# Kernel optimization log

Hardware: AMD Instinct MI355X
Metric: run time of the kernel (lower is better)

## Reference

```python
import jax, jax.numpy as jnp
import numpy as np

HIDDEN = 1024
HEADS = 16
D_K = HIDDEN // HEADS
NEG_INF = -jnp.inf


def setup_inputs() -> dict:
    key = jax.random.key(0)
    ks = jax.random.split(key, 9)
    N, S = 4, 2048
    scale = 1.0 / np.sqrt(HIDDEN)
    x = jax.random.normal(ks[0], (N, S, HIDDEN), dtype=jnp.float32)
    attn_mask = jnp.ones((N, S), dtype=jnp.int32)
    Wq = jax.random.normal(ks[1], (HIDDEN, HIDDEN), dtype=jnp.float32) * scale
    bq = jnp.zeros((HIDDEN,), dtype=jnp.float32)
    Wk = jax.random.normal(ks[2], (HIDDEN, HIDDEN), dtype=jnp.float32) * scale
    bk = jnp.zeros((HIDDEN,), dtype=jnp.float32)
    Wv = jax.random.normal(ks[3], (HIDDEN, HIDDEN), dtype=jnp.float32) * scale
    bv = jnp.zeros((HIDDEN,), dtype=jnp.float32)
    Wp = jax.random.normal(ks[4], (HIDDEN, HIDDEN), dtype=jnp.float32) * scale
    bp = jnp.zeros((HIDDEN,), dtype=jnp.float32)
    return {"x": x, "attn_mask": attn_mask, "Wq": Wq, "bq": bq,
            "Wk": Wk, "bk": bk, "Wv": Wv, "bv": bv, "Wp": Wp, "bp": bp}


def reference(x, attn_mask, Wq, bq, Wk, bk, Wv, bv, Wp, bp):
    N, S, _ = x.shape
    H, dk = HEADS, D_K
    # torch nn.Linear: y = x @ W.T + b
    q = (x @ Wq.T + bq).reshape(N, S, H, dk).transpose(0, 2, 1, 3)  # (N,H,S,dk)
    k = (x @ Wk.T + bk).reshape(N, S, H, dk).transpose(0, 2, 1, 3)
    v = (x @ Wv.T + bv).reshape(N, S, H, dk).transpose(0, 2, 1, 3)
    attn = jnp.einsum('nhqd,nhkd->nhqk', q, k) / jnp.sqrt(jnp.float32(dk))
    mask = attn_mask.reshape(N, 1, 1, S)
    attn = jnp.where(mask == 0, NEG_INF, attn)
    attn = jax.nn.softmax(attn, axis=-1)
    # dropout is identity in eval mode
    y = jnp.einsum('nhqk,nhkd->nhqd', attn, v)  # (N,H,S,dk)
    y = y.transpose(0, 2, 1, 3).reshape(N, S, H * dk)
    return y @ Wp.T + bp
```

## Files before the change

### kernel.cpp

```cpp
#include <hip/hip_runtime.h>

typedef unsigned short u16;
typedef unsigned int u32;
typedef unsigned long long u64;
typedef __attribute__((ext_vector_type(8))) short bf16x8;
typedef __attribute__((ext_vector_type(4))) short bf16x4;
typedef __attribute__((ext_vector_type(4))) float f32x4;
typedef __attribute__((ext_vector_type(2))) unsigned int u32x2;

#define AS1(p) ((const __attribute__((address_space(1))) void*)(p))
#define AS3(p) ((__attribute__((address_space(3))) void*)(p))

__device__ __forceinline__ u16 f2bf(float f) {
    u32 u = __float_as_uint(f);
    u += 0x7fff + ((u >> 16) & 1);
    return (u16)(u >> 16);
}
__device__ __forceinline__ u32 pack2bf(float lo, float hi) {
    u32 a = __float_as_uint(lo) + 0x8000u;
    u32 b = __float_as_uint(hi) + 0x8000u;
    return __builtin_amdgcn_perm(b, a, 0x07060302);
}
__device__ __forceinline__ u32 cvtpk(float lo, float hi) {
    u32 r;
    asm("v_cvt_pk_bf16_f32 %0, %1, %2" : "=v"(r) : "v"(lo), "v"(hi));
    return r;
}

__device__ __forceinline__ void async16(const u16* g, u16* l) {
    __builtin_amdgcn_global_load_lds(AS1(g), AS3(l), 16, 0, 0);
}

__global__ __launch_bounds__(256) void cvt_kernel(const float* __restrict__ src,
                                                  u16* __restrict__ dst, int n) {
    int idx = (blockIdx.x * 256 + threadIdx.x) * 8;
    if (idx >= n) return;
    float4 a = *(const float4*)(src + idx);
    float4 b = *(const float4*)(src + idx + 4);
    uint4 o;
    o.x = (u32)f2bf(a.x) | ((u32)f2bf(a.y) << 16);
    o.y = (u32)f2bf(a.z) | ((u32)f2bf(a.w) << 16);
    o.z = (u32)f2bf(b.x) | ((u32)f2bf(b.y) << 16);
    o.w = (u32)f2bf(b.z) | ((u32)f2bf(b.w) << 16);
    *(uint4*)(dst + idx) = o;
}

__global__ __launch_bounds__(256) void cvt4_kernel(
    const float* __restrict__ s0, const float* __restrict__ s1,
    const float* __restrict__ s2, const float* __restrict__ s3,
    u16* __restrict__ d0, u16* __restrict__ d1,
    u16* __restrict__ d2, u16* __restrict__ d3) {
    const float* s; u16* d;
    switch (blockIdx.y) {
        case 0:  s = s0; d = d0; break;
        case 1:  s = s1; d = d1; break;
        case 2:  s = s2; d = d2; break;
        default: s = s3; d = d3; break;
    }
    int idx = (blockIdx.x * 256 + threadIdx.x) * 8;
    float4 a = *(const float4*)(s + idx);
    float4 b = *(const float4*)(s + idx + 4);
    uint4 o;
    o.x = (u32)f2bf(a.x) | ((u32)f2bf(a.y) << 16);
    o.y = (u32)f2bf(a.z) | ((u32)f2bf(a.w) << 16);
    o.z = (u32)f2bf(b.x) | ((u32)f2bf(b.y) << 16);
    o.w = (u32)f2bf(b.z) | ((u32)f2bf(b.w) << 16);
    *(uint4*)(d + idx) = o;
}

__global__ __launch_bounds__(256, 2) void gemm_bt(
    const u16* __restrict__ A,
    const u16* __restrict__ Wa, const u16* __restrict__ Wb, const u16* __restrict__ Wc,
    const float* __restrict__ ba, const float* __restrict__ bb, const float* __restrict__ bc,
    void* oa, void* ob_, void* oc, int mode)
{
    constexpr int K = 1024;
    __shared__ u16 smem[128 * 132];
    u16* At = smem;
    u16* Wt = smem + 4096;

    const int tid = threadIdx.x;
    const int lane = tid & 63, wv = tid >> 6;
    const int l15 = lane & 15, quad = lane >> 4;
    const int wr = wv >> 1, wc = wv & 1;

    const int L = blockIdx.x + (blockIdx.y << 3) + (blockIdx.z << 9);
    const int g = L & 7;
    const int j = L >> 3;
    const int z = j >> 6;
    const int r = j & 63;
    const int m0 = ((g << 3) + (r & 7)) * 128;
    const int n0 = (r >> 3) * 128;

    const u16* W = (z == 0) ? Wa : ((z == 1) ? Wb : Wc);
    const float* bs = (z == 0) ? ba : ((z == 1) ? bb : bc);
    void* out = (z == 0) ? oa : ((z == 1) ? ob_ : oc);
    const bool swap_ = (mode == 1) || (z < 2);

    f32x4 acc[4][4];
#pragma unroll
    for (int i = 0; i < 4; ++i)
#pragma unroll
        for (int j2 = 0; j2 < 4; ++j2) acc[i][j2] = (f32x4)0.f;

    const int call0 = wv * 2;
    for (int kk = 0; kk < K; kk += 32) {
#pragma unroll
        for (int jj = 0; jj < 2; ++jj) {
            int c = (call0 + jj) * 64 + lane;
            int row = c >> 2;
            int ko = ((c & 3) ^ (row & 3)) * 8;
            async16(A + (size_t)(m0 + row) * K + kk + ko, &At[(call0 + jj) * 512 + lane * 8]);
            async16(W + (size_t)(n0 + row) * K + kk + ko, &Wt[(call0 + jj) * 512 + lane * 8]);
        }
        __syncthreads();

        bf16x8 af[4], wf[4];
#pragma unroll
        for (int t = 0; t < 4; ++t) {
            int rowa = wr * 64 + t * 16 + l15;
            af[t] = *(const bf16x8*)&At[rowa * 32 + ((quad ^ (rowa & 3)) * 8)];
            int rowb = wc * 64 + t * 16 + l15;
            wf[t] = *(const bf16x8*)&Wt[rowb * 32 + ((quad ^ (rowb & 3)) * 8)];
        }
        if (swap_) {
#pragma unroll
            for (int rt = 0; rt < 4; ++rt)
#pragma unroll
                for (int ct = 0; ct < 4; ++ct)
                    acc[rt][ct] = __builtin_amdgcn_mfma_f32_16x16x32_bf16(wf[ct], af[rt], acc[rt][ct], 0, 0, 0);
        } else {
#pragma unroll
            for (int rt = 0; rt < 4; ++rt)
#pragma unroll
                for (int ct = 0; ct < 4; ++ct)
                    acc[rt][ct] = __builtin_amdgcn_mfma_f32_16x16x32_bf16(af[rt], wf[ct], acc[rt][ct], 0, 0, 0);
        }
        __syncthreads();
    }

    if (mode == 1) {
#pragma unroll
        for (int rt = 0; rt < 4; ++rt)
#pragma unroll
            for (int ct = 0; ct < 4; ++ct) {
                int m_ = m0 + wr * 64 + rt * 16 + l15;
                int ob = n0 + wc * 64 + ct * 16 + quad * 4;
                float4 b4 = *(const float4*)&bs[ob];
                float4 v;
                v.x = acc[rt][ct][0] + b4.x;
                v.y = acc[rt][ct][1] + b4.y;
                v.z = acc[rt][ct][2] + b4.z;
                v.w = acc[rt][ct][3] + b4.w;
                *(float4*)((float*)out + (size_t)m_ * 1024 + ob) = v;
            }
        return;
    }

    const int n = m0 >> 11, s0 = m0 & 2047;
    if (z < 2) {
        const float qs = (z == 0) ? 0.18033688011112042f : 1.0f;
#pragma unroll
        for (int rt = 0; rt < 4; ++rt)
#pragma unroll
            for (int ct = 0; ct < 4; ++ct) {
                int ml = wr * 64 + rt * 16 + l15;
                int ol = wc * 64 + ct * 16 + quad * 4;
                float4 b4 = *(const float4*)&bs[n0 + ol];
                float v0 = (acc[rt][ct][0] + b4.x) * qs;
                float v1 = (acc[rt][ct][1] + b4.y) * qs;
                float v2 = (acc[rt][ct][2] + b4.z) * qs;
                float v3 = (acc[rt][ct][3] + b4.w) * qs;
                u32x2 pv = { pack2bf(v0, v1), pack2bf(v2, v3) };
                *(u32x2*)&smem[ml * 132 + ol] = pv;
            }
        __syncthreads();
        const int h0 = n0 >> 6;
#pragma unroll
        for (int p = 0; p < 8; ++p) {
            int hh = p >> 2, qq = p & 3;
            int m = qq * 32 + (tid >> 3), d = (tid & 7) * 8;
            bf16x8 vv = *(const bf16x8*)&smem[m * 132 + hh * 64 + d];
            u16* dst = (u16*)out + ((size_t)((n * 16 + h0 + hh) * 2048 + s0 + m)) * 64 + d;
            *(bf16x8*)dst = vv;
        }
    } else {
#pragma unroll
        for (int rt = 0; rt < 4; ++rt)
#pragma unroll
            for (int ct = 0; ct < 4; ++ct) {
                int ol = wc * 64 + ct * 16 + l15;
                int ml = wr * 64 + rt * 16 + quad * 4;
                float b = bs[n0 + ol];
                float v0 = acc[rt][ct][0] + b;
                float v1 = acc[rt][ct][1] + b;
                float v2 = acc[rt][ct][2] + b;
                float v3 = acc[rt][ct][3] + b;
                u32x2 pv = { pack2bf(v0, v1), pack2bf(v2, v3) };
                *(u32x2*)&smem[ol * 132 + ml] = pv;
            }
        __syncthreads();
#pragma unroll
        for (int p = 0; p < 8; ++p) {
            int o = p * 16 + (tid >> 4), ms = (tid & 15) * 8;
            bf16x8 vv = *(const bf16x8*)&smem[o * 132 + ms];
            int og = n0 + o;
            int h = og >> 6, d = og & 63;
            u16* dst = (u16*)out + ((size_t)((n * 16 + h) * 64 + d)) * 2048 + s0 + ms;
            *(bf16x8*)dst = vv;
        }
    }
}

__global__ __launch_bounds__(256) void attn_kernel(
    const u16* __restrict__ Q, const u16* __restrict__ K_,
    const u16* __restrict__ VT, const int* __restrict__ mask,
    u16* __restrict__ Y)
{
    constexpr int S = 2048, DK = 64, STR = 72;
    __shared__ u16 Kt[64 * STR];
    __shared__ u16 Vt[64 * STR];
    __shared__ int mtile[64];

    const int tid = threadIdx.x;
    const int lane = tid & 63, w = tid >> 6;
    const int l15 = lane & 15, quad = lane >> 4;

    const int L = blockIdx.x + (blockIdx.y << 4);
    const int vb = (L & 7) * 128 + (L >> 3);
    const int nh = vb >> 4;
    const int n = nh >> 4, h = nh & 15;
    const int qbase = (vb & 15) * 128;

    const u16* Qh = Q + (size_t)nh * S * DK;
    const u16* Kh = K_ + (size_t)nh * S * DK;
    const u16* Vh = VT + (size_t)nh * DK * S;

    bf16x8 qf[2][2];
#pragma unroll
    for (int nt = 0; nt < 2; ++nt)
#pragma unroll
        for (int st = 0; st < 2; ++st)
            qf[nt][st] = *(const bf16x8*)(Qh + (size_t)(qbase + w * 32 + nt * 16 + l15) * DK + st * 32 + quad * 8);

    f32x4 o[4][2];
#pragma unroll
    for (int dt = 0; dt < 4; ++dt)
#pragma unroll
        for (int nt = 0; nt < 2; ++nt) o[dt][nt] = (f32x4)0.f;
    float lsum[2] = {0.f, 0.f};

    const int r0 = tid >> 3, c8 = (tid & 7) * 8;
    bf16x8 rk0 = *(const bf16x8*)(Kh + (size_t)r0 * 64 + c8);
    bf16x8 rk1 = *(const bf16x8*)(Kh + (size_t)(r0 + 32) * 64 + c8);
    bf16x8 rv0 = *(const bf16x8*)(Vh + (size_t)r0 * S + c8);
    bf16x8 rv1 = *(const bf16x8*)(Vh + (size_t)(r0 + 32) * S + c8);
    int mreg = 0;
    if (tid < 64) mreg = mask[n * S + tid];

    for (int it = 0; it < 32; ++it) {
        *(bf16x8*)&Kt[r0 * STR + c8] = rk0;
        *(bf16x8*)&Kt[(r0 + 32) * STR + c8] = rk1;
        *(bf16x8*)&Vt[r0 * STR + c8] = rv0;
        *(bf16x8*)&Vt[(r0 + 32) * STR + c8] = rv1;
        if (tid < 64) mtile[tid] = mreg;
        __syncthreads();

        const int kkn = ((it + 1) << 6) & (S - 1);
        rk0 = *(const bf16x8*)(Kh + (size_t)(kkn + r0) * 64 + c8);
        rk1 = *(const bf16x8*)(Kh + (size_t)(kkn + r0 + 32) * 64 + c8);
        rv0 = *(const bf16x8*)(Vh + (size_t)r0 * S + kkn + c8);
        rv1 = *(const bf16x8*)(Vh + (size_t)(r0 + 32) * S + kkn + c8);
        if (tid < 64) mreg = mask[n * S + kkn + tid];

        f32x4 sacc[4][2];
#pragma unroll
        for (int jt = 0; jt < 4; ++jt)
#pragma unroll
            for (int nt = 0; nt < 2; ++nt) sacc[jt][nt] = (f32x4)0.f;
        __builtin_amdgcn_s_setprio(1);
#pragma unroll
        for (int st = 0; st < 2; ++st)
#pragma unroll
            for (int jt = 0; jt < 4; ++jt) {
                bf16x8 kf = *(const bf16x8*)&Kt[(jt * 16 + l15) * STR + st * 32 + quad * 8];
                sacc[jt][0] = __builtin_amdgcn_mfma_f32_16x16x32_bf16(kf, qf[0][st], sacc[jt][0], 0, 0, 0);
                sacc[jt][1] = __builtin_amdgcn_mfma_f32_16x16x32_bf16(kf, qf[1][st], sacc[jt][1], 0, 0, 0);
            }
        __builtin_amdgcn_s_setprio(0);

        const bool fast = (__ballot(mtile[lane] != 0) == ~0ull);
        if (!fast) {
#pragma unroll
            for (int jt = 0; jt < 4; ++jt)
#pragma unroll
                for (int r = 0; r < 4; ++r) {
                    int mv = mtile[jt * 16 + quad * 4 + r];
#pragma unroll
                    for (int nt = 0; nt < 2; ++nt)
                        if (mv == 0) sacc[jt][nt][r] = -1e30f;
                }
        }

        bf16x8 pb[2][2];
#pragma unroll
        for (int nt = 0; nt < 2; ++nt) {
            float ps = 0.f;
            u32 pkx[4], pky[4];
#pragma unroll
            for (int jt = 0; jt < 4; ++jt) {
                float e0 = __builtin_amdgcn_exp2f(sacc[jt][nt][0]);
                float e1 = __builtin_amdgcn_exp2f(sacc[jt][nt][1]);
                float e2 = __builtin_amdgcn_exp2f(sacc[jt][nt][2]);
                float e3 = __builtin_amdgcn_exp2f(sacc[jt][nt][3]);
                ps += (e0 + e1) + (e2 + e3);
                pkx[jt] = cvtpk(e0, e1);
                pky[jt] = cvtpk(e2, e3);
            }
            lsum[nt] += ps;
#pragma unroll
            for (int kt = 0; kt < 2; ++kt) {
                auto rX = __builtin_amdgcn_permlane32_swap(pkx[2 * kt], pkx[2 * kt + 1], false, false);
                auto rY = __builtin_amdgcn_permlane32_swap(pky[2 * kt], pky[2 * kt + 1], false, false);
                auto sX = __builtin_amdgcn_permlane16_swap(rX[0], rX[1], false, false);
                auto sY = __builtin_amdgcn_permlane16_swap(rY[0], rY[1], false, false);
                union { u32 u[4]; bf16x8 v; } pu;
                pu.u[0] = sX[0];
                pu.u[1] = sY[0];
                pu.u[2] = sX[1];
                pu.u[3] = sY[1];
                pb[nt][kt] = pu.v;
            }
        }

        __builtin_amdgcn_s_setprio(1);
#pragma unroll
        for (int kt = 0; kt < 2; ++kt) {
#pragma unroll
            for (int dt = 0; dt < 4; ++dt) {
                bf16x8 vf = *(const bf16x8*)&Vt[(dt * 16 + l15) * STR + kt * 32 + quad * 8];
                o[dt][0] = __builtin_amdgcn_mfma_f32_16x16x32_bf16(vf, pb[0][kt], o[dt][0], 0, 0, 0);
                o[dt][1] = __builtin_amdgcn_mfma_f32_16x16x32_bf16(vf, pb[1][kt], o[dt][1], 0, 0, 0);
            }
        }
        __builtin_amdgcn_s_setprio(0);
        __syncthreads();
    }

#pragma unroll
    for (int nt = 0; nt < 2; ++nt) {
        float ls = lsum[nt];
        ls += __shfl_xor(ls, 16);
        ls += __shfl_xor(ls, 32);
        float rl = (ls > 0.f) ? 1.f / ls : 0.f;
        int qi = qbase + w * 32 + nt * 16 + l15;
#pragma unroll
        for (int dt = 0; dt < 4; ++dt) {
            u32x2 pv = { pack2bf(o[dt][nt][0] * rl, o[dt][nt][1] * rl),
                         pack2bf(o[dt][nt][2] * rl, o[dt][nt][3] * rl) };
            size_t base = ((size_t)(n * 2048 + qi)) * 1024 + h * 64 + dt * 16 + quad * 4;
            *(u32x2*)(Y + base) = pv;
        }
    }
}

extern "C" void kernel_launch(void* const* d_in, const int* in_sizes, int n_in,
                              void* d_out, int out_size, void* d_ws, size_t ws_size,
                              hipStream_t stream) {
    const float* x  = (const float*)d_in[0];
    const int* mask = (const int*)d_in[1];
    const float* Wq = (const float*)d_in[2];
    const float* bq = (const float*)d_in[3];
    const float* Wk = (const float*)d_in[4];
    const float* bk = (const float*)d_in[5];
    const float* Wv = (const float*)d_in[6];
    const float* bv = (const float*)d_in[7];
    const float* Wp = (const float*)d_in[8];
    const float* bp = (const float*)d_in[9];

    char* ws = (char*)d_ws;
    u16* xb  = (u16*)(ws);
    u16* wqb = (u16*)(ws + (16u << 20));
    u16* wkb = (u16*)(ws + (18u << 20));
    u16* wvb = (u16*)(ws + (20u << 20));
    u16* wpb = (u16*)(ws + (22u << 20));
    u16* Qb  = (u16*)(ws + (24u << 20));
    u16* Kb  = (u16*)(ws + (40u << 20));
    u16* Vb  = (u16*)(ws + (56u << 20));
    u16* Yb  = (u16*)(ws + (72u << 20));

    cvt_kernel<<<4096, 256, 0, stream>>>(x, xb, 8388608);
    cvt4_kernel<<<dim3(512, 4), 256, 0, stream>>>(Wq, Wk, Wv, Wp, wqb, wkb, wvb, wpb);

    gemm_bt<<<dim3(8, 64, 3), 256, 0, stream>>>(xb, wqb, wkb, wvb, bq, bk, bv,
                                                (void*)Qb, (void*)Kb, (void*)Vb, 0);

    attn_kernel<<<dim3(16, 64), 256, 0, stream>>>(Qb, Kb, Vb, mask, Yb);

    gemm_bt<<<dim3(8, 64, 1), 256, 0, stream>>>(Yb, wpb, wpb, wpb, bp, bp, bp,
                                                d_out, d_out, d_out, 1);
}
```

Baseline: 304.2 us.

## Double-buffer K/V tiles in LDS to drop one barrier per iteration

The attention loop now uses two LDS buffers for the K, V and mask tiles. The next tile's LDS writes go into the other buffer during the current iteration, so each iteration needs only one __syncthreads instead of two. The first QK MFMA now takes a zero constant as its accumulator rather than a separately zeroed array. In exchange, LDS use doubles, which may lower occupancy, and global loads are now issued later within the iteration.

```diff
diff --git a/kernel.cpp b/kernel.cpp
--- a/kernel.cpp
+++ b/kernel.cpp
@@ -218,9 +218,9 @@
     u16* __restrict__ Y)
 {
     constexpr int S = 2048, DK = 64, STR = 72;
-    __shared__ u16 Kt[64 * STR];
-    __shared__ u16 Vt[64 * STR];
-    __shared__ int mtile[64];
+    __shared__ u16 Kt[2][64 * STR];
+    __shared__ u16 Vt[2][64 * STR];
+    __shared__ int mtile[2][64];
 
     const int tid = threadIdx.x;
     const int lane = tid & 63, w = tid >> 6;
@@ -251,51 +251,58 @@
     float lsum[2] = {0.f, 0.f};
 
     const int r0 = tid >> 3, c8 = (tid & 7) * 8;
-    bf16x8 rk0 = *(const bf16x8*)(Kh + (size_t)r0 * 64 + c8);
-    bf16x8 rk1 = *(const bf16x8*)(Kh + (size_t)(r0 + 32) * 64 + c8);
-    bf16x8 rv0 = *(const bf16x8*)(Vh + (size_t)r0 * S + c8);
-    bf16x8 rv1 = *(const bf16x8*)(Vh + (size_t)(r0 + 32) * S + c8);
-    int mreg = 0;
-    if (tid < 64) mreg = mask[n * S + tid];
+
+    {
+        bf16x8 k0 = *(const bf16x8*)(Kh + (size_t)r0 * 64 + c8);
+        bf16x8 k1 = *(const bf16x8*)(Kh + (size_t)(r0 + 32) * 64 + c8);
+        bf16x8 v0 = *(const bf16x8*)(Vh + (size_t)r0 * S + c8);
+        bf16x8 v1 = *(const bf16x8*)(Vh + (size_t)(r0 + 32) * S + c8);
+        *(bf16x8*)&Kt[0][r0 * STR + c8] = k0;
+        *(bf16x8*)&Kt[0][(r0 + 32) * STR + c8] = k1;
+        *(bf16x8*)&Vt[0][r0 * STR + c8] = v0;
+        *(bf16x8*)&Vt[0][(r0 + 32) * STR + c8] = v1;
+        if (tid < 64) mtile[0][tid] = mask[n * S + tid];
+    }
+    __syncthreads();
+
+    const f32x4 zf = (f32x4)0.f;
 
     for (int it = 0; it < 32; ++it) {
-        *(bf16x8*)&Kt[r0 * STR + c8] = rk0;
-        *(bf16x8*)&Kt[(r0 + 32) * STR + c8] = rk1;
-        *(bf16x8*)&Vt[r0 * STR + c8] = rv0;
-        *(bf16x8*)&Vt[(r0 + 32) * STR + c8] = rv1;
-        if (tid < 64) mtile[tid] = mreg;
-        __syncthreads();
+        const int cur = it & 1, nxt = cur ^ 1;
+        const u16* Ktc = &Kt[cur][0];
+        const u16* Vtc = &Vt[cur][0];
 
         const int kkn = ((it + 1) << 6) & (S - 1);
-        rk0 = *(const bf16x8*)(Kh + (size_t)(kkn + r0) * 64 + c8);
-        rk1 = *(const bf16x8*)(Kh + (size_t)(kkn + r0 + 32) * 64 + c8);
-        rv0 = *(const bf16x8*)(Vh + (size_t)r0 * S + kkn + c8);
-        rv1 = *(const bf16x8*)(Vh + (size_t)(r0 + 32) * S + kkn + c8);
+        bf16x8 rk0 = *(const bf16x8*)(Kh + (size_t)(kkn + r0) * 64 + c8);
+        bf16x8 rk1 = *(const bf16x8*)(Kh + (size_t)(kkn + r0 + 32) * 64 + c8);
+        bf16x8 rv0 = *(const bf16x8*)(Vh + (size_t)r0 * S + kkn + c8);
+        bf16x8 rv1 = *(const bf16x8*)(Vh + (size_t)(r0 + 32) * S + kkn + c8);
+        int mreg = 0;
         if (tid < 64) mreg = mask[n * S + kkn + tid];
 
         f32x4 sacc[4][2];
-#pragma unroll
-        for (int jt = 0; jt < 4; ++jt)
-#pragma unroll
-            for (int nt = 0; nt < 2; ++nt) sacc[jt][nt] = (f32x4)0.f;
         __builtin_amdgcn_s_setprio(1);
 #pragma unroll
-        for (int st = 0; st < 2; ++st)
-#pragma unroll
-            for (int jt = 0; jt < 4; ++jt) {
-                bf16x8 kf = *(const bf16x8*)&Kt[(jt * 16 + l15) * STR + st * 32 + quad * 8];
-                sacc[jt][0] = __builtin_amdgcn_mfma_f32_16x16x32_bf16(kf, qf[0][st], sacc[jt][0], 0, 0, 0);
-                sacc[jt][1] = __builtin_amdgcn_mfma_f32_16x16x32_bf16(kf, qf[1][st], sacc[jt][1], 0, 0, 0);
-            }
+        for (int jt = 0; jt < 4; ++jt) {
+            bf16x8 kf = *(const bf16x8*)&Ktc[(jt * 16 + l15) * STR + quad * 8];
+            sacc[jt][0] = __builtin_amdgcn_mfma_f32_16x16x32_bf16(kf, qf[0][0], zf, 0, 0, 0);
+            sacc[jt][1] = __builtin_amdgcn_mfma_f32_16x16x32_bf16(kf, qf[1][0], zf, 0, 0, 0);
+        }
+#pragma unroll
+        for (int jt = 0; jt < 4; ++jt) {
+            bf16x8 kf = *(const bf16x8*)&Ktc[(jt * 16 + l15) * STR + 32 + quad * 8];
+            sacc[jt][0] = __builtin_amdgcn_mfma_f32_16x16x32_bf16(kf, qf[0][1], sacc[jt][0], 0, 0, 0);
+            sacc[jt][1] = __builtin_amdgcn_mfma_f32_16x16x32_bf16(kf, qf[1][1], sacc[jt][1], 0, 0, 0);
+        }
         __builtin_amdgcn_s_setprio(0);
 
-        const bool fast = (__ballot(mtile[lane] != 0) == ~0ull);
+        const bool fast = (__ballot(mtile[cur][lane] != 0) == ~0ull);
         if (!fast) {
 #pragma unroll
             for (int jt = 0; jt < 4; ++jt)
 #pragma unroll
                 for (int r = 0; r < 4; ++r) {
-                    int mv = mtile[jt * 16 + quad * 4 + r];
+                    int mv = mtile[cur][jt * 16 + quad * 4 + r];
 #pragma unroll
                     for (int nt = 0; nt < 2; ++nt)
                         if (mv == 0) sacc[jt][nt][r] = -1e30f;
@@ -333,17 +340,24 @@
             }
         }
 
+        *(bf16x8*)&Kt[nxt][r0 * STR + c8] = rk0;
+        *(bf16x8*)&Kt[nxt][(r0 + 32) * STR + c8] = rk1;
+        *(bf16x8*)&Vt[nxt][r0 * STR + c8] = rv0;
+        *(bf16x8*)&Vt[nxt][(r0 + 32) * STR + c8] = rv1;
+        if (tid < 64) mtile[nxt][tid] = mreg;
+
         __builtin_amdgcn_s_setprio(1);
 #pragma unroll
         for (int kt = 0; kt < 2; ++kt) {
 #pragma unroll
             for (int dt = 0; dt < 4; ++dt) {
-                bf16x8 vf = *(const bf16x8*)&Vt[(dt * 16 + l15) * STR + kt * 32 + quad * 8];
+                bf16x8 vf = *(const bf16x8*)&Vtc[(dt * 16 + l15) * STR + kt * 32 + quad * 8];
                 o[dt][0] = __builtin_amdgcn_mfma_f32_16x16x32_bf16(vf, pb[0][kt], o[dt][0], 0, 0, 0);
                 o[dt][1] = __builtin_amdgcn_mfma_f32_16x16x32_bf16(vf, pb[1][kt], o[dt][1], 0, 0, 0);
             }
         }
         __builtin_amdgcn_s_setprio(0);
+
         __syncthreads();
     }
 
```

Result: no change. 303.8 us (-0.1%).
